# Performance work log

Hardware: AMD Instinct MI355X
Metric: run time of the kernel (lower is better)

The kernel has to match this reference:

```python
import jax, jax.numpy as jnp
import numpy as np

N = 20000   # nodes
E = 320000  # edges (before self-loops)
HID = 64    # hidden_dim
H = 4       # attention heads
C = HID     # per-head channels (concat=False -> mean over heads)
CDIM = 8    # contrastive_dim
NEG_SLOPE = 0.2


def setup_inputs() -> dict:
    key = jax.random.key(0)
    ks = jax.random.split(key, 32)
    g = lambda k, shape: (jax.random.normal(k, shape, jnp.float32) * 0.05)
    inp = {
        "x": jax.random.normal(ks[0], (N, 8), jnp.float32),
        "edge_index": jax.random.randint(ks[1], (2, E), 0, N, jnp.int64),
        # lc_encode MLP: 8 -> 32 -> HID
        "W_enc1": g(ks[2], (8, 32)),  "b_enc1": jnp.zeros((32,), jnp.float32),
        "W_enc2": g(ks[3], (32, HID)), "b_enc2": jnp.zeros((HID,), jnp.float32),
        # three GATConv layers: lin (HID -> H*C, no bias), att_src/att_dst (H, C), bias (C,)
        "W_g1": g(ks[4], (HID, H * C)), "as1": g(ks[5], (H, C)), "ad1": g(ks[6], (H, C)), "bg1": jnp.zeros((C,), jnp.float32),
        "W_g2": g(ks[7], (HID, H * C)), "as2": g(ks[8], (H, C)), "ad2": g(ks[9], (H, C)), "bg2": jnp.zeros((C,), jnp.float32),
        "W_g3": g(ks[10], (HID, H * C)), "as3": g(ks[11], (H, C)), "ad3": g(ks[12], (H, C)), "bg3": jnp.zeros((C,), jnp.float32),
        # output MLP: HID -> 64 -> 32 -> CDIM (dropout inactive at eval)
        "W_o1": g(ks[13], (HID, 64)), "b_o1": jnp.zeros((64,), jnp.float32),
        "W_o2": g(ks[14], (64, 32)),  "b_o2": jnp.zeros((32,), jnp.float32),
        "W_o3": g(ks[15], (32, CDIM)), "b_o3": jnp.zeros((CDIM,), jnp.float32),
    }
    return inp


def gat_conv(x, src, dst, n, W, att_src, att_dst, bias):
    # PyG GATConv, heads=H, concat=False (mean over heads), eval mode (no dropout)
    h = (x @ W).reshape(n, H, C)                       # [N,H,C]
    a_src = jnp.einsum('nhc,hc->nh', h, att_src)        # [N,H]
    a_dst = jnp.einsum('nhc,hc->nh', h, att_dst)        # [N,H]
    logits = jax.nn.leaky_relu(a_src[src] + a_dst[dst], NEG_SLOPE)  # [Etot,H]
    m = jax.ops.segment_max(logits, dst, num_segments=n)            # segment softmax (stable)
    e = jnp.exp(logits - m[dst])
    denom = jax.ops.segment_sum(e, dst, num_segments=n)
    alpha = e / (denom[dst] + 1e-16)                    # [Etot,H]
    msg = h[src] * alpha[:, :, None]                    # [Etot,H,C]
    out = jax.ops.segment_sum(msg, dst, num_segments=n) # [N,H,C]
    return out.mean(axis=1) + bias                      # concat=False -> head mean


def reference(x, edge_index, W_enc1, b_enc1, W_enc2, b_enc2,
              W_g1, as1, ad1, bg1, W_g2, as2, ad2, bg2, W_g3, as3, ad3, bg3,
              W_o1, b_o1, W_o2, b_o2, W_o3, b_o3):
    n = x.shape[0]
    loops = jnp.arange(n, dtype=edge_index.dtype)       # GATConv add_self_loops=True
    src = jnp.concatenate([edge_index[0], loops])
    dst = jnp.concatenate([edge_index[1], loops])

    h = jax.nn.elu(jax.nn.elu(x @ W_enc1 + b_enc1) @ W_enc2 + b_enc2)
    h1 = gat_conv(h, src, dst, n, W_g1, as1, ad1, bg1) + h
    h2 = gat_conv(h1, src, dst, n, W_g2, as2, ad2, bg2) + h1
    h3 = gat_conv(h2, src, dst, n, W_g3, as3, ad3, bg3) + h2

    o = jax.nn.elu(h3 @ W_o1 + b_o1)
    o = jax.nn.elu(o @ W_o2 + b_o2)
    return o @ W_o3 + b_o3
```

## Files before the change

### kernel.cpp

```cpp
#include <hip/hip_runtime.h>
#include <cstdint>
#include <cstddef>

#define NEG_SLOPE 0.2f

__device__ __forceinline__ float elu_f(float x) {
    return x > 0.f ? x : expm1f(x);
}

__global__ __launch_bounds__(256) void prep_kernel(
    const int* __restrict__ ei,
    const float* __restrict__ W0, const float* __restrict__ as0, const float* __restrict__ ad0,
    const float* __restrict__ W1, const float* __restrict__ as1, const float* __restrict__ ad1,
    const float* __restrict__ W2, const float* __restrict__ as2, const float* __restrict__ ad2,
    int* __restrict__ cnt, int* __restrict__ ready, int* __restrict__ flag,
    float* __restrict__ vfold, int n) {
    const int b = blockIdx.x, t = threadIdx.x;
    if (b < 79) {
        const int i = b * 256 + t;
        if (i < n) cnt[i] = 0;
        if (b == 0) {
            if (t < 128) ready[t] = 0;
            if (t == 0) {
                int acc = 0;
#pragma unroll
                for (int k = 0; k < 8; ++k) acc |= ei[2 * k + 1];
                flag[0] = (acc == 0) ? 1 : 0;
            }
        }
        return;
    }
    const int e = (b - 79) * 256 + t;
    if (e >= 1536) return;
    const int l = e >> 9, rem = e & 511;
    const int k = rem >> 3, j = rem & 7, h = j & 3;
    const float* W   = (l == 0) ? W0  : (l == 1) ? W1  : W2;
    const float* as_ = (l == 0) ? as0 : (l == 1) ? as1 : as2;
    const float* ad_ = (l == 0) ? ad0 : (l == 1) ? ad1 : ad2;
    const float* av = (j < 4) ? as_ : ad_;
    const float* wr = W + k * 256 + h * 64;
    const float* ar = av + h * 64;
    float s = 0.f;
#pragma unroll 8
    for (int cc = 0; cc < 64; ++cc) s += wr[cc] * ar[cc];
    vfold[l * 512 + k * 8 + j] = s;
}

__global__ void count_kernel(const int* __restrict__ ei, const int* __restrict__ flag,
                             int E, int Etot, int* __restrict__ cnt) {
    int e = blockIdx.x * blockDim.x + threadIdx.x;
    if (e >= Etot) return;
    int d;
    if (e < E) d = flag[0] ? ei[2 * (size_t)(E + e)] : ei[E + e];
    else       d = e - E;
    atomicAdd(&cnt[d], 1);
}

#define SCAN_B 256
__global__ __launch_bounds__(256) void scan_onepass_kernel(
    const int* __restrict__ cnt, int* __restrict__ ready,
    int* __restrict__ rowptr, int* __restrict__ cursor, int n) {
    __shared__ int sd[SCAN_B];
    __shared__ int sred[128];
    __shared__ int s_pref;
    const int b = blockIdx.x, t = threadIdx.x;
    const int g = b * SCAN_B + t;
    const int v = (g < n) ? cnt[g] : 0;
    sd[t] = v;
    __syncthreads();
    for (int off = 1; off < SCAN_B; off <<= 1) {
        int add = (t >= off) ? sd[t - off] : 0;
        __syncthreads();
        sd[t] += add;
        __syncthreads();
    }
    if (t == SCAN_B - 1) atomicExch(&ready[b], sd[SCAN_B - 1] + 1);
    if (t < 128) {
        int pv = 0;
        if (t < b) {
            do { pv = atomicAdd(&ready[t], 0); __builtin_amdgcn_s_sleep(1); } while (pv == 0);
            pv -= 1;
        }
        sred[t] = pv;
    }
    __syncthreads();
    if (t == 0) {
        int s = 0;
#pragma unroll 8
        for (int i = 0; i < 128; ++i) s += sred[i];
        s_pref = s;
    }
    __syncthreads();
    const int pre = s_pref;
    if (g < n) {
        const int e = pre + sd[t];
        rowptr[g + 1] = e;
        cursor[g] = e - v;
        if (g == 0) rowptr[0] = 0;
// ... 94 lines not shown
    float o[4][4];
#pragma unroll
    for (int i = 0; i < 4; ++i)
#pragma unroll
        for (int c = 0; c < 4; ++c) o[i][c] = elu_f(acc[i][c]);

#pragma unroll
    for (int i = 0; i < 4; ++i) {
        const int n = n0 + nq * 4 + i;
        if (n < n_nodes)
            *(float4*)(h0 + (size_t)n * 64 + c0) =
                make_float4(o[i][0], o[i][1], o[i][2], o[i][3]);
    }
    float ad[4][8];
#pragma unroll
    for (int i = 0; i < 4; ++i)
#pragma unroll
        for (int jj = 0; jj < 8; ++jj) ad[i][jj] = 0.f;
#pragma unroll
    for (int c = 0; c < 4; ++c) {
        const float4 v0 = *(const float4*)(vsd + (c0 + c) * 8);
        const float4 v1 = *(const float4*)(vsd + (c0 + c) * 8 + 4);
#pragma unroll
        for (int i = 0; i < 4; ++i) {
            ad[i][0] += o[i][c] * v0.x; ad[i][1] += o[i][c] * v0.y;
            ad[i][2] += o[i][c] * v0.z; ad[i][3] += o[i][c] * v0.w;
            ad[i][4] += o[i][c] * v1.x; ad[i][5] += o[i][c] * v1.y;
            ad[i][6] += o[i][c] * v1.z; ad[i][7] += o[i][c] * v1.w;
        }
    }
#pragma unroll
    for (int off = 1; off < 16; off <<= 1) {
#pragma unroll
        for (int i = 0; i < 4; ++i)
#pragma unroll
            for (int jj = 0; jj < 8; ++jj)
                ad[i][jj] += __shfl_xor(ad[i][jj], off);
    }
    if (cg == 0) {
#pragma unroll
        for (int i = 0; i < 4; ++i) {
            const int n = n0 + nq * 4 + i;
            if (n < n_nodes) {
#pragma unroll
                for (int h = 0; h < 4; ++h) {
                    asrc[n * 4 + h] = ad[i][h];
                    adst[n * 4 + h] = ad[i][4 + h];
                }
            }
        }
    }
}

#define GSTR 132
__global__ __launch_bounds__(512, 2) void gat_fused_kernel(
    const float* __restrict__ bin, const float* __restrict__ asrc,
    const float* __restrict__ adst, const int* __restrict__ rowptr,
    const int* __restrict__ col,
    const float* __restrict__ W, const float* __restrict__ bias,
    const float* __restrict__ vfold_next, int has_next,
    float* __restrict__ out,
    float* __restrict__ nasrc, float* __restrict__ nadst,
    const float* __restrict__ Wm1, const float* __restrict__ bm1,
    const float* __restrict__ Wm2, const float* __restrict__ bm2,
    const float* __restrict__ Wm3, const float* __restrict__ bm3,
    float* __restrict__ mlp_out, int n_nodes) {
    __shared__ float gS[64 * GSTR];
    __shared__ float Wp[4096];
    __shared__ float vN[512];
    const int t = threadIdx.x;
    const int n0 = blockIdx.x * 64;
    const int grp = t >> 4;
    const int q = t & 15;
    const int c0 = q * 4;

    if (has_next && t < 128) *(float4*)(vN + t * 4) = *(const float4*)(vfold_next + t * 4);

    float keep[2][8];
#pragma unroll
    for (int i = 0; i < 2; ++i) {
        const int nl = grp * 2 + i;
        const int n = n0 + nl;
        float acc[4][4];
#pragma unroll
        for (int h = 0; h < 4; ++h)
#pragma unroll
            for (int z = 0; z < 4; ++z) acc[h][z] = 0.f;
        if (n < n_nodes) {
            float4 den4 = make_float4(0.f, 0.f, 0.f, 0.f);
            const float4 ad4 = *(const float4*)(adst + (size_t)n * 4);
            const int start = rowptr[n], end = rowptr[n + 1];
            for (int base = start; base < end; base += 16) {
                const int cnt = min(16, end - base);
                int c = 0;
                float4 w4 = make_float4(0.f, 0.f, 0.f, 0.f);
                if (base + q < end) {
                    c = col[base + q];
                    const float4 av = *(const float4*)(asrc + (size_t)c * 4);
                    float l0 = av.x + ad4.x; l0 = l0 > 0.f ? l0 : NEG_SLOPE * l0;
                    float l1 = av.y + ad4.y; l1 = l1 > 0.f ? l1 : NEG_SLOPE * l1;
                    float l2 = av.z + ad4.z; l2 = l2 > 0.f ? l2 : NEG_SLOPE * l2;
                    float l3 = av.w + ad4.w; l3 = l3 > 0.f ? l3 : NEG_SLOPE * l3;
                    w4.x = __expf(fminf(l0, 60.f));
                    w4.y = __expf(fminf(l1, 60.f));
                    w4.z = __expf(fminf(l2, 60.f));
                    w4.w = __expf(fminf(l3, 60.f));
                    den4.x += w4.x; den4.y += w4.y; den4.z += w4.z; den4.w += w4.w;
                }
                int j = 0;
                for (; j + 4 <= cnt; j += 4) {
#pragma unroll
                    for (int u = 0; u < 4; ++u) {
                        const int s = __shfl(c, j + u, 16);
                        const float4 hv = *(const float4*)(bin + (size_t)s * 64 + q * 4);
                        const float wx = __shfl(w4.x, j + u, 16);
                        const float wy = __shfl(w4.y, j + u, 16);
                        const float wz = __shfl(w4.z, j + u, 16);
                        const float ww = __shfl(w4.w, j + u, 16);
                        acc[0][0] += wx * hv.x; acc[0][1] += wx * hv.y;
                        acc[0][2] += wx * hv.z; acc[0][3] += wx * hv.w;
                        acc[1][0] += wy * hv.x; acc[1][1] += wy * hv.y;
                        acc[1][2] += wy * hv.z; acc[1][3] += wy * hv.w;
                        acc[2][0] += wz * hv.x; acc[2][1] += wz * hv.y;
                        acc[2][2] += wz * hv.z; acc[2][3] += wz * hv.w;
                        acc[3][0] += ww * hv.x; acc[3][1] += ww * hv.y;
                        acc[3][2] += ww * hv.z; acc[3][3] += ww * hv.w;
                    }
                }
                for (; j < cnt; ++j) {
                    const int s = __shfl(c, j, 16);
                    const float4 hv = *(const float4*)(bin + (size_t)s * 64 + q * 4);
                    const float wx = __shfl(w4.x, j, 16);
                    const float wy = __shfl(w4.y, j, 16);
                    const float wz = __shfl(w4.z, j, 16);
                    const float ww = __shfl(w4.w, j, 16);
                    acc[0][0] += wx * hv.x; acc[0][1] += wx * hv.y;
                    acc[0][2] += wx * hv.z; acc[0][3] += wx * hv.w;
                    acc[1][0] += wy * hv.x; acc[1][1] += wy * hv.y;
                    acc[1][2] += wy * hv.z; acc[1][3] += wy * hv.w;
                    acc[2][0] += wz * hv.x; acc[2][1] += wz * hv.y;
                    acc[2][2] += wz * hv.z; acc[2][3] += wz * hv.w;
                    acc[3][0] += ww * hv.x; acc[3][1] += ww * hv.y;
                    acc[3][2] += ww * hv.z; acc[3][3] += ww * hv.w;
                }
            }
#pragma unroll
            for (int off = 1; off < 16; off <<= 1) {
                den4.x += __shfl_xor(den4.x, off, 16);
                den4.y += __shfl_xor(den4.y, off, 16);
                den4.z += __shfl_xor(den4.z, off, 16);
                den4.w += __shfl_xor(den4.w, off, 16);
            }
            const float i0 = 1.f / (den4.x + 1e-16f);
            const float i1 = 1.f / (den4.y + 1e-16f);
            const float i2 = 1.f / (den4.z + 1e-16f);
            const float i3 = 1.f / (den4.w + 1e-16f);
            *(float4*)(gS + nl * GSTR + c0) =
                make_float4(acc[0][0] * i0, acc[0][1] * i0, acc[0][2] * i0, acc[0][3] * i0);
            *(float4*)(gS + nl * GSTR + 64 + c0) =
                make_float4(acc[1][0] * i1, acc[1][1] * i1, acc[1][2] * i1, acc[1][3] * i1);
            keep[i][0] = acc[2][0] * i2; keep[i][1] = acc[2][1] * i2;
            keep[i][2] = acc[2][2] * i2; keep[i][3] = acc[2][3] * i2;
            keep[i][4] = acc[3][0] * i3; keep[i][5] = acc[3][1] * i3;
            keep[i][6] = acc[3][2] * i3; keep[i][7] = acc[3][3] * i3;
        } else {
            const float4 z4 = make_float4(0.f, 0.f, 0.f, 0.f);
            *(float4*)(gS + nl * GSTR + c0) = z4;
            *(float4*)(gS + nl * GSTR + 64 + c0) = z4;
#pragma unroll
            for (int u = 0; u < 8; ++u) keep[i][u] = 0.f;
        }
    }

    float ga2[2][4];
#pragma unroll
    for (int i = 0; i < 2; ++i)
#pragma unroll
        for (int c = 0; c < 4; ++c) ga2[i][c] = 0.f;

#pragma unroll
    for (int half = 0; half < 2; ++half) {
        if (half == 1) {
#pragma unroll
            for (int i = 0; i < 2; ++i) {
                const int nl = grp * 2 + i;
                *(float4*)(gS + nl * GSTR + c0) =
                    make_float4(keep[i][0], keep[i][1], keep[i][2], keep[i][3]);
                *(float4*)(gS + nl * GSTR + 64 + c0) =
                    make_float4(keep[i][4], keep[i][5], keep[i][6], keep[i][7]);
            }
        }
#pragma unroll
        for (int s = 0; s < 2; ++s) {
#pragma unroll
            for (int j = 0; j < 2; ++j) {
                const int f4 = j * 512 + t;
                const int kl = f4 >> 4;
                const int c = (f4 & 15) * 4;
                const int m = half * 128 + s * 64 + kl;
                const int h = m >> 6, kk = m & 63;
                *(float4*)(Wp + kl * 64 + c) = *(const float4*)(W + kk * 256 + h * 64 + c);
            }
            __syncthreads();
#pragma unroll 4
            for (int ks = 0; ks < 64; ks += 4) {
                const float4 a0 = *(const float4*)(gS + (grp * 2 + 0) * GSTR + s * 64 + ks);
                const float4 a1 = *(const float4*)(gS + (grp * 2 + 1) * GSTR + s * 64 + ks);
                const float4 w0 = *(const float4*)(Wp + (ks + 0) * 64 + c0);
                const float4 w1 = *(const float4*)(Wp + (ks + 1) * 64 + c0);
                const float4 w2 = *(const float4*)(Wp + (ks + 2) * 64 + c0);
                const float4 w3 = *(const float4*)(Wp + (ks + 3) * 64 + c0);
                ga2[0][0] += a0.x * w0.x + a0.y * w1.x + a0.z * w2.x + a0.w * w3.x;
                ga2[0][1] += a0.x * w0.y + a0.y * w1.y + a0.z * w2.y + a0.w * w3.y;
                ga2[0][2] += a0.x * w0.z + a0.y * w1.z + a0.z * w2.z + a0.w * w3.z;
                ga2[0][3] += a0.x * w0.w + a0.y * w1.w + a0.z * w2.w + a0.w * w3.w;
                ga2[1][0] += a1.x * w0.x + a1.y * w1.x + a1.z * w2.x + a1.w * w3.x;
                ga2[1][1] += a1.x * w0.y + a1.y * w1.y + a1.z * w2.y + a1.w * w3.y;
                ga2[1][2] += a1.x * w0.z + a1.y * w1.z + a1.z * w2.z + a1.w * w3.z;
                ga2[1][3] += a1.x * w0.w + a1.y * w1.w + a1.z * w2.w + a1.w * w3.w;
            }
            __syncthreads();
        }
    }

    const float4 bb = *(const float4*)(bias + c0);
    float o[2][4];
#pragma unroll
    for (int i = 0; i < 2; ++i) {
        const int n = n0 + grp * 2 + i;
        if (n < n_nodes) {
            const float4 x4 = *(const float4*)(bin + (size_t)n * 64 + c0);
            o[i][0] = 0.25f * ga2[i][0] + bb.x + x4.x;
            o[i][1] = 0.25f * ga2[i][1] + bb.y + x4.y;
            o[i][2] = 0.25f * ga2[i][2] + bb.z + x4.z;
            o[i][3] = 0.25f * ga2[i][3] + bb.w + x4.w;
            if (has_next)
                *(float4*)(out + (size_t)n * 64 + c0) =
                    make_float4(o[i][0], o[i][1], o[i][2], o[i][3]);
        } else {
            o[i][0] = o[i][1] = o[i][2] = o[i][3] = 0.f;
        }
    }

    if (has_next) {
        float pj[2][8];
#pragma unroll
        for (int i = 0; i < 2; ++i)
#pragma unroll
            for (int jj = 0; jj < 8; ++jj) pj[i][jj] = 0.f;
#pragma unroll
        for (int c = 0; c < 4; ++c) {
            const float4 v0 = *(const float4*)(vN + (c0 + c) * 8);
            const float4 v1 = *(const float4*)(vN + (c0 + c) * 8 + 4);
#pragma unroll
            for (int i = 0; i < 2; ++i) {
                pj[i][0] += o[i][c] * v0.x; pj[i][1] += o[i][c] * v0.y;
                pj[i][2] += o[i][c] * v0.z; pj[i][3] += o[i][c] * v0.w;
                pj[i][4] += o[i][c] * v1.x; pj[i][5] += o[i][c] * v1.y;
                pj[i][6] += o[i][c] * v1.z; pj[i][7] += o[i][c] * v1.w;
            }
        }
#pragma unroll
        for (int off = 1; off < 16; off <<= 1) {
#pragma unroll
            for (int i = 0; i < 2; ++i)
#pragma unroll
                for (int jj = 0; jj < 8; ++jj)
                    pj[i][jj] += __shfl_xor(pj[i][jj], off);
        }
        if (q == 0) {
#pragma unroll
            for (int i = 0; i < 2; ++i) {
                const int n = n0 + grp * 2 + i;
                if (n < n_nodes) {
#pragma unroll
                    for (int h = 0; h < 4; ++h) {
                        nasrc[n * 4 + h] = pj[i][h];
                        nadst[n * 4 + h] = pj[i][4 + h];
                    }
                }
            }
        }
        return;
    }

#pragma unroll
    for (int i = 0; i < 2; ++i)
        *(float4*)(gS + (grp * 2 + i) * GSTR + c0) =
            make_float4(o[i][0], o[i][1], o[i][2], o[i][3]);
#pragma unroll
    for (int j = 0; j < 2; ++j)
        *(float4*)(Wp + (j * 512 + t) * 4) = *(const float4*)(Wm1 + (j * 512 + t) * 4);
    if (t < 64) vN[t] = bm1[t];
    else if (t < 96) vN[t] = bm2[t - 64];
    else if (t < 104) vN[t] = bm3[t - 96];
    if (t < 256) vN[104 + t] = Wm3[t];
    __syncthreads();
    {
        const int ng = t >> 3;
        const int cm0 = (t & 7) * 8;
        float a1[8];
#pragma unroll
        for (int u = 0; u < 8; ++u) a1[u] = vN[cm0 + u];
#pragma unroll 4
        for (int k = 0; k < 64; ++k) {
            const float hv = gS[ng * GSTR + k];
            const float4 w0 = *(const float4*)(Wp + k * 64 + cm0);
            const float4 w1 = *(const float4*)(Wp + k * 64 + cm0 + 4);
            a1[0] += hv * w0.x; a1[1] += hv * w0.y;
            a1[2] += hv * w0.z; a1[3] += hv * w0.w;
            a1[4] += hv * w1.x; a1[5] += hv * w1.y;
            a1[6] += hv * w1.z; a1[7] += hv * w1.w;
        }
        *(float4*)(gS + ng * GSTR + 64 + cm0) =
            make_float4(elu_f(a1[0]), elu_f(a1[1]), elu_f(a1[2]), elu_f(a1[3]));
        *(float4*)(gS + ng * GSTR + 64 + cm0 + 4) =
            make_float4(elu_f(a1[4]), elu_f(a1[5]), elu_f(a1[6]), elu_f(a1[7]));
    }
    __syncthreads();
    *(float4*)(Wp + t * 4) = *(const float4*)(Wm2 + t * 4);
    __syncthreads();
    {
        const int nn = t >> 3;
        const int cc0 = (t & 7) * 4;
        float a2[4];
#pragma unroll
        for (int u = 0; u < 4; ++u) a2[u] = vN[64 + cc0 + u];
#pragma unroll 4
        for (int j = 0; j < 64; ++j) {
            const float ov = gS[nn * GSTR + 64 + j];
            const float4 w = *(const float4*)(Wp + j * 32 + cc0);
            a2[0] += ov * w.x; a2[1] += ov * w.y;
            a2[2] += ov * w.z; a2[3] += ov * w.w;
        }
        __syncthreads();
        *(float4*)(gS + nn * GSTR + cc0) =
            make_float4(elu_f(a2[0]), elu_f(a2[1]), elu_f(a2[2]), elu_f(a2[3]));
    }
    __syncthreads();
    {
        const int nl = t >> 3;
        const int c3 = t & 7;
        const int n = n0 + nl;
        if (n < n_nodes) {
            float a3 = vN[96 + c3];
#pragma unroll 4
            for (int j = 0; j < 32; ++j)
                a3 += gS[nl * GSTR + j] * vN[104 + j * 8 + c3];
            mlp_out[(size_t)n * 8 + c3] = a3;
        }
    }
}

extern "C" void kernel_launch(void* const* d_in, const int* in_sizes, int n_in,
                              void* d_out, int out_size, void* d_ws, size_t ws_size,
                              hipStream_t stream) {
    const float* x     = (const float*)d_in[0];
    const int*   ei    = (const int*)d_in[1];
    const float* Wenc1 = (const float*)d_in[2];
    const float* benc1 = (const float*)d_in[3];
    const float* Wenc2 = (const float*)d_in[4];
    const float* benc2 = (const float*)d_in[5];
    const float* Wg[3]  = {(const float*)d_in[6],  (const float*)d_in[10], (const float*)d_in[14]};
    const float* as_[3] = {(const float*)d_in[7],  (const float*)d_in[11], (const float*)d_in[15]};
    const float* ad_[3] = {(const float*)d_in[8],  (const float*)d_in[12], (const float*)d_in[16]};
    const float* bg[3]  = {(const float*)d_in[9],  (const float*)d_in[13], (const float*)d_in[17]};
    const float* Wo1 = (const float*)d_in[18];
    const float* bo1 = (const float*)d_in[19];
    const float* Wo2 = (const float*)d_in[20];
    const float* bo2 = (const float*)d_in[21];
    const float* Wo3 = (const float*)d_in[22];
    const float* bo3 = (const float*)d_in[23];

    const int N = in_sizes[0] / 8;
    const int E = in_sizes[1] / 2;
    const int Etot = E + N;
    const int nblk = (N + SCAN_B - 1) / SCAN_B;
    const int FB = (Etot + 255) / 256;
    const int NB64 = (N + 63) / 64;

    float* buf0  = (float*)d_ws;
    float* buf1  = buf0 + (size_t)N * 64;
    float* asA   = buf1 + (size_t)N * 64;
    float* adA   = asA + (size_t)N * 4;
    float* asB   = adA + (size_t)N * 4;
    float* adB   = asB + (size_t)N * 4;
    float* vfold = adB + (size_t)N * 4;
    int* rowptr = (int*)(vfold + 3 * 512);
    int* cursor = rowptr + (N + 2);
    int* cnt    = cursor + N;
    int* ready  = cnt + N;
    int* flag   = ready + 128;
    int* col    = flag + 2;

    prep_kernel<<<nblk + 6, 256, 0, stream>>>(ei,
        Wg[0], as_[0], ad_[0], Wg[1], as_[1], ad_[1], Wg[2], as_[2], ad_[2],
        cnt, ready, flag, vfold, N);
    count_kernel<<<(Etot + 255) / 256, 256, 0, stream>>>(ei, flag, E, Etot, cnt);
    scan_onepass_kernel<<<nblk, SCAN_B, 0, stream>>>(cnt, ready, rowptr, cursor, N);
    fillenc_kernel<<<FB + NB64, 256, 0, stream>>>(ei, flag, E, Etot, cursor, col, FB,
                                                  x, Wenc1, benc1, Wenc2, benc2,
                                                  vfold, buf0, asA, adA, N);

    gat_fused_kernel<<<NB64, 512, 0, stream>>>(
        buf0, asA, adA, rowptr, col, Wg[0], bg[0], vfold + 512, 1,
        buf1, asB, adB, Wo1, bo1, Wo2, bo2, Wo3, bo3, (float*)d_out, N);
    gat_fused_kernel<<<NB64, 512, 0, stream>>>(
        buf1, asB, adB, rowptr, col, Wg[1], bg[1], vfold + 1024, 1,
        buf0, asA, adA, Wo1, bo1, Wo2, bo2, Wo3, bo3, (float*)d_out, N);
    gat_fused_kernel<<<NB64, 512, 0, stream>>>(
        buf0, asA, adA, rowptr, col, Wg[2], bg[2], vfold, 0,
        buf1, asB, adB, Wo1, bo1, Wo2, bo2, Wo3, bo3, (float*)d_out, N);
}
```

Baseline: 282.0 us.

## Halve GAT node tile to one node per thread group and raise occupancy bound

Each fused GAT block now covers 32 nodes instead of 64. Every 16-thread group aggregates one node's neighbours rather than two, which doubles the grid and should spread the latency-bound gather across more CUs. The dense projection and MLP tail run on only half the threads, and the launch bound asks for 8 blocks per CU. That bound may force a tight register budget and cause spills, while the idle half of the block wastes lanes during the GEMM phase.

Measured after the change: 281.8 us (median of 3 runs). Within noise of the previous version (-0.1%).

```diff
diff --git a/kernel.cpp b/kernel.cpp
--- a/kernel.cpp
+++ b/kernel.cpp
@@ -245,7 +245,7 @@
 }
 
 #define GSTR 132
-__global__ __launch_bounds__(512, 2) void gat_fused_kernel(
+__global__ __launch_bounds__(512, 8) void gat_fused_kernel(
     const float* __restrict__ bin, const float* __restrict__ asrc,
     const float* __restrict__ adst, const int* __restrict__ rowptr,
     const int* __restrict__ col,
@@ -257,22 +257,20 @@
     const float* __restrict__ Wm2, const float* __restrict__ bm2,
     const float* __restrict__ Wm3, const float* __restrict__ bm3,
     float* __restrict__ mlp_out, int n_nodes) {
-    __shared__ float gS[64 * GSTR];
+    __shared__ float gS[32 * GSTR];
     __shared__ float Wp[4096];
     __shared__ float vN[512];
     const int t = threadIdx.x;
-    const int n0 = blockIdx.x * 64;
+    const int n0 = blockIdx.x * 32;
     const int grp = t >> 4;
     const int q = t & 15;
     const int c0 = q * 4;
 
     if (has_next && t < 128) *(float4*)(vN + t * 4) = *(const float4*)(vfold_next + t * 4);
 
-    float keep[2][8];
-#pragma unroll
-    for (int i = 0; i < 2; ++i) {
-        const int nl = grp * 2 + i;
-        const int n = n0 + nl;
+    float keep[8];
+    {
+        const int n = n0 + grp;
         float acc[4][4];
 #pragma unroll
         for (int h = 0; h < 4; ++h)
@@ -347,23 +345,24 @@
             const float i1 = 1.f / (den4.y + 1e-16f);
             const float i2 = 1.f / (den4.z + 1e-16f);
             const float i3 = 1.f / (den4.w + 1e-16f);
-            *(float4*)(gS + nl * GSTR + c0) =
+            *(float4*)(gS + grp * GSTR + c0) =
                 make_float4(acc[0][0] * i0, acc[0][1] * i0, acc[0][2] * i0, acc[0][3] * i0);
-            *(float4*)(gS + nl * GSTR + 64 + c0) =
+            *(float4*)(gS + grp * GSTR + 64 + c0) =
                 make_float4(acc[1][0] * i1, acc[1][1] * i1, acc[1][2] * i1, acc[1][3] * i1);
-            keep[i][0] = acc[2][0] * i2; keep[i][1] = acc[2][1] * i2;
-            keep[i][2] = acc[2][2] * i2; keep[i][3] = acc[2][3] * i2;
-            keep[i][4] = acc[3][0] * i3; keep[i][5] = acc[3][1] * i3;
-            keep[i][6] = acc[3][2] * i3; keep[i][7] = acc[3][3] * i3;
+            keep[0] = acc[2][0] * i2; keep[1] = acc[2][1] * i2;
+            keep[2] = acc[2][2] * i2; keep[3] = acc[2][3] * i2;
+            keep[4] = acc[3][0] * i3; keep[5] = acc[3][1] * i3;
+            keep[6] = acc[3][2] * i3; keep[7] = acc[3][3] * i3;
         } else {
             const float4 z4 = make_float4(0.f, 0.f, 0.f, 0.f);
-            *(float4*)(gS + nl * GSTR + c0) = z4;
-            *(float4*)(gS + nl * GSTR + 64 + c0) = z4;
-#pragma unroll
-            for (int u = 0; u < 8; ++u) keep[i][u] = 0.f;
-        }
-    }
-
+            *(float4*)(gS + grp * GSTR + c0) = z4;
+            *(float4*)(gS + grp * GSTR + 64 + c0) = z4;
+#pragma unroll
+            for (int u = 0; u < 8; ++u) keep[u] = 0.f;
+        }
+    }
+
+    const int ng2 = t >> 4;
     float ga2[2][4];
 #pragma unroll
     for (int i = 0; i < 2; ++i)
@@ -373,14 +372,10 @@
 #pragma unroll
     for (int half = 0; half < 2; ++half) {
         if (half == 1) {
-#pragma unroll
-            for (int i = 0; i < 2; ++i) {
-                const int nl = grp * 2 + i;
-                *(float4*)(gS + nl * GSTR + c0) =
-                    make_float4(keep[i][0], keep[i][1], keep[i][2], keep[i][3]);
-                *(float4*)(gS + nl * GSTR + 64 + c0) =
-                    make_float4(keep[i][4], keep[i][5], keep[i][6], keep[i][7]);
-            }
+            *(float4*)(gS + grp * GSTR + c0) =
+                make_float4(keep[0], keep[1], keep[2], keep[3]);
+            *(float4*)(gS + grp * GSTR + 64 + c0) =
+                make_float4(keep[4], keep[5], keep[6], keep[7]);
         }
 #pragma unroll
         for (int s = 0; s < 2; ++s) {
@@ -394,81 +389,91 @@
                 *(float4*)(Wp + kl * 64 + c) = *(const float4*)(W + kk * 256 + h * 64 + c);
             }
             __syncthreads();
+            if (t < 256) {
 #pragma unroll 4
-            for (int ks = 0; ks < 64; ks += 4) {
-                const float4 a0 = *(const float4*)(gS + (grp * 2 + 0) * GSTR + s * 64 + ks);
-                const float4 a1 = *(const float4*)(gS + (grp * 2 + 1) * GSTR + s * 64 + ks);
-                const float4 w0 = *(const float4*)(Wp + (ks + 0) * 64 + c0);
-                const float4 w1 = *(const float4*)(Wp + (ks + 1) * 64 + c0);
-                const float4 w2 = *(const float4*)(Wp + (ks + 2) * 64 + c0);
-                const float4 w3 = *(const float4*)(Wp + (ks + 3) * 64 + c0);
-                ga2[0][0] += a0.x * w0.x + a0.y * w1.x + a0.z * w2.x + a0.w * w3.x;
-                ga2[0][1] += a0.x * w0.y + a0.y * w1.y + a0.z * w2.y + a0.w * w3.y;
-                ga2[0][2] += a0.x * w0.z + a0.y * w1.z + a0.z * w2.z + a0.w * w3.z;
-                ga2[0][3] += a0.x * w0.w + a0.y * w1.w + a0.z * w2.w + a0.w * w3.w;
-                ga2[1][0] += a1.x * w0.x + a1.y * w1.x + a1.z * w2.x + a1.w * w3.x;
-                ga2[1][1] += a1.x * w0.y + a1.y * w1.y + a1.z * w2.y + a1.w * w3.y;
-                ga2[1][2] += a1.x * w0.z + a1.y * w1.z + a1.z * w2.z + a1.w * w3.z;
-                ga2[1][3] += a1.x * w0.w + a1.y * w1.w + a1.z * w2.w + a1.w * w3.w;
+                for (int ks = 0; ks < 64; ks += 4) {
+                    const float4 a0 = *(const float4*)(gS + (ng2 * 2 + 0) * GSTR + s * 64 + ks);
+                    const float4 a1 = *(const float4*)(gS + (ng2 * 2 + 1) * GSTR + s * 64 + ks);
+                    const float4 w0 = *(const float4*)(Wp + (ks + 0) * 64 + c0);
+                    const float4 w1 = *(const float4*)(Wp + (ks + 1) * 64 + c0);
+                    const float4 w2 = *(const float4*)(Wp + (ks + 2) * 64 + c0);
+                    const float4 w3 = *(const float4*)(Wp + (ks + 3) * 64 + c0);
+                    ga2[0][0] += a0.x * w0.x + a0.y * w1.x + a0.z * w2.x + a0.w * w3.x;
+                    ga2[0][1] += a0.x * w0.y + a0.y * w1.y + a0.z * w2.y + a0.w * w3.y;
+                    ga2[0][2] += a0.x * w0.z + a0.y * w1.z + a0.z * w2.z + a0.w * w3.z;
+                    ga2[0][3] += a0.x * w0.w + a0.y * w1.w + a0.z * w2.w + a0.w * w3.w;
+                    ga2[1][0] += a1.x * w0.x + a1.y * w1.x + a1.z * w2.x + a1.w * w3.x;
+                    ga2[1][1] += a1.x * w0.y + a1.y * w1.y + a1.z * w2.y + a1.w * w3.y;
+                    ga2[1][2] += a1.x * w0.z + a1.y * w1.z + a1.z * w2.z + a1.w * w3.z;
+                    ga2[1][3] += a1.x * w0.w + a1.y * w1.w + a1.z * w2.w + a1.w * w3.w;
+                }
             }
             __syncthreads();
         }
     }
 
-    const float4 bb = *(const float4*)(bias + c0);
     float o[2][4];
-#pragma unroll
-    for (int i = 0; i < 2; ++i) {
-        const int n = n0 + grp * 2 + i;
-        if (n < n_nodes) {
-            const float4 x4 = *(const float4*)(bin + (size_t)n * 64 + c0);
-            o[i][0] = 0.25f * ga2[i][0] + bb.x + x4.x;
-            o[i][1] = 0.25f * ga2[i][1] + bb.y + x4.y;
-            o[i][2] = 0.25f * ga2[i][2] + bb.z + x4.z;
-            o[i][3] = 0.25f * ga2[i][3] + bb.w + x4.w;
-            if (has_next)
-                *(float4*)(out + (size_t)n * 64 + c0) =
-                    make_float4(o[i][0], o[i][1], o[i][2], o[i][3]);
-        } else {
+    if (t < 256) {
+        const float4 bb = *(const float4*)(bias + c0);
+#pragma unroll
+        for (int i = 0; i < 2; ++i) {
+            const int n = n0 + ng2 * 2 + i;
+            if (n < n_nodes) {
+                const float4 x4 = *(const float4*)(bin + (size_t)n * 64 + c0);
+                o[i][0] = 0.25f * ga2[i][0] + bb.x + x4.x;
+                o[i][1] = 0.25f * ga2[i][1] + bb.y + x4.y;
+                o[i][2] = 0.25f * ga2[i][2] + bb.z + x4.z;
+                o[i][3] = 0.25f * ga2[i][3] + bb.w + x4.w;
+                if (has_next)
+                    *(float4*)(out + (size_t)n * 64 + c0) =
+                        make_float4(o[i][0], o[i][1], o[i][2], o[i][3]);
+            } else {
+                o[i][0] = o[i][1] = o[i][2] = o[i][3] = 0.f;
+            }
+        }
+    } else {
+#pragma unroll
+        for (int i = 0; i < 2; ++i)
             o[i][0] = o[i][1] = o[i][2] = o[i][3] = 0.f;
-        }
     }
 
     if (has_next) {
-        float pj[2][8];
-#pragma unroll
-        for (int i = 0; i < 2; ++i)
-#pragma unroll
-            for (int jj = 0; jj < 8; ++jj) pj[i][jj] = 0.f;
-#pragma unroll
-        for (int c = 0; c < 4; ++c) {
-            const float4 v0 = *(const float4*)(vN + (c0 + c) * 8);
-            const float4 v1 = *(const float4*)(vN + (c0 + c) * 8 + 4);
-#pragma unroll
-            for (int i = 0; i < 2; ++i) {
-                pj[i][0] += o[i][c] * v0.x; pj[i][1] += o[i][c] * v0.y;
-                pj[i][2] += o[i][c] * v0.z; pj[i][3] += o[i][c] * v0.w;
-                pj[i][4] += o[i][c] * v1.x; pj[i][5] += o[i][c] * v1.y;
-                pj[i][6] += o[i][c] * v1.z; pj[i][7] += o[i][c] * v1.w;
-            }
-        }
-#pragma unroll
-        for (int off = 1; off < 16; off <<= 1) {
+        if (t < 256) {
+            float pj[2][8];
 #pragma unroll
             for (int i = 0; i < 2; ++i)
 #pragma unroll
-                for (int jj = 0; jj < 8; ++jj)
-                    pj[i][jj] += __shfl_xor(pj[i][jj], off);
-        }
-        if (q == 0) {
-#pragma unroll
-            for (int i = 0; i < 2; ++i) {
-                const int n = n0 + grp * 2 + i;
-                if (n < n_nodes) {
-#pragma unroll
-                    for (int h = 0; h < 4; ++h) {
-                        nasrc[n * 4 + h] = pj[i][h];
-                        nadst[n * 4 + h] = pj[i][4 + h];
+                for (int jj = 0; jj < 8; ++jj) pj[i][jj] = 0.f;
+#pragma unroll
+            for (int c = 0; c < 4; ++c) {
+                const float4 v0 = *(const float4*)(vN + (c0 + c) * 8);
+                const float4 v1 = *(const float4*)(vN + (c0 + c) * 8 + 4);
+#pragma unroll
+                for (int i = 0; i < 2; ++i) {
+                    pj[i][0] += o[i][c] * v0.x; pj[i][1] += o[i][c] * v0.y;
+                    pj[i][2] += o[i][c] * v0.z; pj[i][3] += o[i][c] * v0.w;
+                    pj[i][4] += o[i][c] * v1.x; pj[i][5] += o[i][c] * v1.y;
+                    pj[i][6] += o[i][c] * v1.z; pj[i][7] += o[i][c] * v1.w;
+                }
+            }
+#pragma unroll
+            for (int off = 1; off < 16; off <<= 1) {
+#pragma unroll
+                for (int i = 0; i < 2; ++i)
+#pragma unroll
+                    for (int jj = 0; jj < 8; ++jj)
+                        pj[i][jj] += __shfl_xor(pj[i][jj], off);
+            }
+            if (q == 0) {
+#pragma unroll
+                for (int i = 0; i < 2; ++i) {
+                    const int n = n0 + ng2 * 2 + i;
+                    if (n < n_nodes) {
+#pragma unroll
+                        for (int h = 0; h < 4; ++h) {
+                            nasrc[n * 4 + h] = pj[i][h];
+                            nadst[n * 4 + h] = pj[i][4 + h];
+                        }
                     }
                 }
             }
@@ -476,10 +481,12 @@
         return;
     }
 
-#pragma unroll
-    for (int i = 0; i < 2; ++i)
-        *(float4*)(gS + (grp * 2 + i) * GSTR + c0) =
-            make_float4(o[i][0], o[i][1], o[i][2], o[i][3]);
+    if (t < 256) {
+#pragma unroll
+        for (int i = 0; i < 2; ++i)
+            *(float4*)(gS + (ng2 * 2 + i) * GSTR + c0) =
+                make_float4(o[i][0], o[i][1], o[i][2], o[i][3]);
+    }
 #pragma unroll
     for (int j = 0; j < 2; ++j)
         *(float4*)(Wp + (j * 512 + t) * 4) = *(const float4*)(Wm1 + (j * 512 + t) * 4);
@@ -488,7 +495,7 @@
     else if (t < 104) vN[t] = bm3[t - 96];
     if (t < 256) vN[104 + t] = Wm3[t];
     __syncthreads();
-    {
+    if (t < 256) {
         const int ng = t >> 3;
         const int cm0 = (t & 7) * 8;
         float a1[8];
@@ -512,7 +519,7 @@
     __syncthreads();
     *(float4*)(Wp + t * 4) = *(const float4*)(Wm2 + t * 4);
     __syncthreads();
-    {
+    if (t < 256) {
         const int nn = t >> 3;
         const int cc0 = (t & 7) * 4;
         float a2[4];
@@ -528,9 +535,11 @@
         __syncthreads();
         *(float4*)(gS + nn * GSTR + cc0) =
             make_float4(elu_f(a2[0]), elu_f(a2[1]), elu_f(a2[2]), elu_f(a2[3]));
-    }
-    __syncthreads();
-    {
+    } else {
+        __syncthreads();
+    }
+    __syncthreads();
+    if (t < 256) {
         const int nl = t >> 3;
         const int c3 = t & 7;
         const int n = n0 + nl;
@@ -570,6 +579,7 @@
     const int nblk = (N + SCAN_B - 1) / SCAN_B;
     const int FB = (Etot + 255) / 256;
     const int NB64 = (N + 63) / 64;
+    const int NB32 = (N + 31) / 32;
 
     float* buf0  = (float*)d_ws;
     float* buf1  = buf0 + (size_t)N * 64;
@@ -594,13 +604,13 @@
                                                   x, Wenc1, benc1, Wenc2, benc2,
                                                   vfold, buf0, asA, adA, N);
 
-    gat_fused_kernel<<<NB64, 512, 0, stream>>>(
+    gat_fused_kernel<<<NB32, 512, 0, stream>>>(
         buf0, asA, adA, rowptr, col, Wg[0], bg[0], vfold + 512, 1,
         buf1, asB, adB, Wo1, bo1, Wo2, bo2, Wo3, bo3, (float*)d_out, N);
-    gat_fused_kernel<<<NB64, 512, 0, stream>>>(
+    gat_fused_kernel<<<NB32, 512, 0, stream>>>(
         buf1, asB, adB, rowptr, col, Wg[1], bg[1], vfold + 1024, 1,
         buf0, asA, adA, Wo1, bo1, Wo2, bo2, Wo3, bo3, (float*)d_out, N);
-    gat_fused_kernel<<<NB64, 512, 0, stream>>>(
+    gat_fused_kernel<<<NB32, 512, 0, stream>>>(
         buf0, asA, adA, rowptr, col, Wg[2], bg[2], vfold, 0,
         buf1, asB, adB, Wo1, bo1, Wo2, bo2, Wo3, bo3, (float*)d_out, N);
 }
```

## Pre-transpose GAT weights and stream them from global in fused layer kernel

Applied to the files above, without the earlier changes.

The prep kernel now writes a transposed, per-wave-sliced copy of each GAT weight matrix. The fused layer kernel stores all four head aggregates in an XOR-swizzled shared tile and has each wave compute 8 output channels for 64 nodes, reading weights straight from global or L2 instead of staging them through shared memory in halves. Each lane now recomputes attention weights per edge instead of exchanging them by shuffle. Dropping the weight buffer and shuffles is meant to cut LDS use and barriers so the launch bound can rise to 4 blocks per CU. The cost is a larger gS tile and more redundant exp and asrc loads per edge.

Measured after the change: 300.1 us. 6.4% more time.

```diff
diff --git a/kernel.cpp b/kernel.cpp
--- a/kernel.cpp
+++ b/kernel.cpp
@@ -14,7 +14,7 @@
     const float* __restrict__ W1, const float* __restrict__ as1, const float* __restrict__ ad1,
     const float* __restrict__ W2, const float* __restrict__ as2, const float* __restrict__ ad2,
     int* __restrict__ cnt, int* __restrict__ ready, int* __restrict__ flag,
-    float* __restrict__ vfold, int n) {
+    float* __restrict__ vfold, float* __restrict__ wt, int n) {
     const int b = blockIdx.x, t = threadIdx.x;
     if (b < 79) {
         const int i = b * 256 + t;
@@ -30,20 +30,32 @@
         }
         return;
     }
-    const int e = (b - 79) * 256 + t;
-    if (e >= 1536) return;
-    const int l = e >> 9, rem = e & 511;
-    const int k = rem >> 3, j = rem & 7, h = j & 3;
-    const float* W   = (l == 0) ? W0  : (l == 1) ? W1  : W2;
-    const float* as_ = (l == 0) ? as0 : (l == 1) ? as1 : as2;
-    const float* ad_ = (l == 0) ? ad0 : (l == 1) ? ad1 : ad2;
-    const float* av = (j < 4) ? as_ : ad_;
-    const float* wr = W + k * 256 + h * 64;
-    const float* ar = av + h * 64;
-    float s = 0.f;
+    if (b < 85) {
+        const int e = (b - 79) * 256 + t;
+        if (e >= 1536) return;
+        const int l = e >> 9, rem = e & 511;
+        const int k = rem >> 3, j = rem & 7, h = j & 3;
+        const float* W   = (l == 0) ? W0  : (l == 1) ? W1  : W2;
+        const float* as_ = (l == 0) ? as0 : (l == 1) ? as1 : as2;
+        const float* ad_ = (l == 0) ? ad0 : (l == 1) ? ad1 : ad2;
+        const float* av = (j < 4) ? as_ : ad_;
+        const float* wr = W + k * 256 + h * 64;
+        const float* ar = av + h * 64;
+        float s = 0.f;
 #pragma unroll 8
-    for (int cc = 0; cc < 64; ++cc) s += wr[cc] * ar[cc];
-    vfold[l * 512 + k * 8 + j] = s;
+        for (int cc = 0; cc < 64; ++cc) s += wr[cc] * ar[cc];
+        vfold[l * 512 + k * 8 + j] = s;
+        return;
+    }
+    const int idx = (b - 85) * 256 + t;
+    if (idx >= 3 * 16384) return;
+    const int l = idx >> 14;
+    const int r = idx & 16383;
+    const float* W = (l == 0) ? W0 : (l == 1) ? W1 : W2;
+    const int w = r >> 11;
+    const int kap = (r >> 3) & 255;
+    const int c = r & 7;
+    wt[idx] = W[(kap & 63) * 256 + (kap >> 6) * 64 + w * 8 + c];
 }
 
 __global__ void count_kernel(const int* __restrict__ ei, const int* __restrict__ flag,
@@ -244,12 +256,12 @@
     }
 }
 
-#define GSTR 132
-__global__ __launch_bounds__(512, 2) void gat_fused_kernel(
+#define GSTR 264
+__global__ __launch_bounds__(512, 4) void gat_fused_kernel(
     const float* __restrict__ bin, const float* __restrict__ asrc,
     const float* __restrict__ adst, const int* __restrict__ rowptr,
     const int* __restrict__ col,
-    const float* __restrict__ W, const float* __restrict__ bias,
+    const float* __restrict__ Wt, const float* __restrict__ bias,
     const float* __restrict__ vfold_next, int has_next,
     float* __restrict__ out,
     float* __restrict__ nasrc, float* __restrict__ nadst,
@@ -258,21 +270,19 @@
     const float* __restrict__ Wm3, const float* __restrict__ bm3,
     float* __restrict__ mlp_out, int n_nodes) {
     __shared__ float gS[64 * GSTR];
-    __shared__ float Wp[4096];
     __shared__ float vN[512];
     const int t = threadIdx.x;
     const int n0 = blockIdx.x * 64;
     const int grp = t >> 4;
     const int q = t & 15;
-    const int c0 = q * 4;
 
     if (has_next && t < 128) *(float4*)(vN + t * 4) = *(const float4*)(vfold_next + t * 4);
 
-    float keep[2][8];
 #pragma unroll
     for (int i = 0; i < 2; ++i) {
         const int nl = grp * 2 + i;
         const int n = n0 + nl;
+        const int sw = nl & 7;
         float acc[4][4];
 #pragma unroll
         for (int h = 0; h < 4; ++h)
@@ -285,191 +295,132 @@
             for (int base = start; base < end; base += 16) {
                 const int cnt = min(16, end - base);
                 int c = 0;
-                float4 w4 = make_float4(0.f, 0.f, 0.f, 0.f);
-                if (base + q < end) {
-                    c = col[base + q];
-                    const float4 av = *(const float4*)(asrc + (size_t)c * 4);
+                if (base + q < end) c = col[base + q];
+#pragma unroll 4
+                for (int j = 0; j < cnt; ++j) {
+                    const int s = __shfl(c, j, 16);
+                    const float4 av = *(const float4*)(asrc + (size_t)s * 4);
+                    const float4 hv = *(const float4*)(bin + (size_t)s * 64 + q * 4);
                     float l0 = av.x + ad4.x; l0 = l0 > 0.f ? l0 : NEG_SLOPE * l0;
                     float l1 = av.y + ad4.y; l1 = l1 > 0.f ? l1 : NEG_SLOPE * l1;
                     float l2 = av.z + ad4.z; l2 = l2 > 0.f ? l2 : NEG_SLOPE * l2;
                     float l3 = av.w + ad4.w; l3 = l3 > 0.f ? l3 : NEG_SLOPE * l3;
-                    w4.x = __expf(fminf(l0, 60.f));
-                    w4.y = __expf(fminf(l1, 60.f));
-                    w4.z = __expf(fminf(l2, 60.f));
-                    w4.w = __expf(fminf(l3, 60.f));
-                    den4.x += w4.x; den4.y += w4.y; den4.z += w4.z; den4.w += w4.w;
-                }
-                int j = 0;
-                for (; j + 4 <= cnt; j += 4) {
-#pragma unroll
-                    for (int u = 0; u < 4; ++u) {
-                        const int s = __shfl(c, j + u, 16);
-                        const float4 hv = *(const float4*)(bin + (size_t)s * 64 + q * 4);
-                        const float wx = __shfl(w4.x, j + u, 16);
-                        const float wy = __shfl(w4.y, j + u, 16);
-                        const float wz = __shfl(w4.z, j + u, 16);
-                        const float ww = __shfl(w4.w, j + u, 16);
-                        acc[0][0] += wx * hv.x; acc[0][1] += wx * hv.y;
-                        acc[0][2] += wx * hv.z; acc[0][3] += wx * hv.w;
-                        acc[1][0] += wy * hv.x; acc[1][1] += wy * hv.y;
-                        acc[1][2] += wy * hv.z; acc[1][3] += wy * hv.w;
-                        acc[2][0] += wz * hv.x; acc[2][1] += wz * hv.y;
-                        acc[2][2] += wz * hv.z; acc[2][3] += wz * hv.w;
-                        acc[3][0] += ww * hv.x; acc[3][1] += ww * hv.y;
-                        acc[3][2] += ww * hv.z; acc[3][3] += ww * hv.w;
-                    }
-                }
-                for (; j < cnt; ++j) {
-                    const int s = __shfl(c, j, 16);
-                    const float4 hv = *(const float4*)(bin + (size_t)s * 64 + q * 4);
-                    const float wx = __shfl(w4.x, j, 16);
-                    const float wy = __shfl(w4.y, j, 16);
-                    const float wz = __shfl(w4.z, j, 16);
-                    const float ww = __shfl(w4.w, j, 16);
-                    acc[0][0] += wx * hv.x; acc[0][1] += wx * hv.y;
-                    acc[0][2] += wx * hv.z; acc[0][3] += wx * hv.w;
-                    acc[1][0] += wy * hv.x; acc[1][1] += wy * hv.y;
-                    acc[1][2] += wy * hv.z; acc[1][3] += wy * hv.w;
-                    acc[2][0] += wz * hv.x; acc[2][1] += wz * hv.y;
-                    acc[2][2] += wz * hv.z; acc[2][3] += wz * hv.w;
-                    acc[3][0] += ww * hv.x; acc[3][1] += ww * hv.y;
-                    acc[3][2] += ww * hv.z; acc[3][3] += ww * hv.w;
+                    const float w0 = __expf(fminf(l0, 60.f));
+                    const float w1 = __expf(fminf(l1, 60.f));
+                    const float w2 = __expf(fminf(l2, 60.f));
+                    const float w3 = __expf(fminf(l3, 60.f));
+                    den4.x += w0; den4.y += w1; den4.z += w2; den4.w += w3;
+                    acc[0][0] += w0 * hv.x; acc[0][1] += w0 * hv.y;
+                    acc[0][2] += w0 * hv.z; acc[0][3] += w0 * hv.w;
+                    acc[1][0] += w1 * hv.x; acc[1][1] += w1 * hv.y;
+                    acc[1][2] += w1 * hv.z; acc[1][3] += w1 * hv.w;
+                    acc[2][0] += w2 * hv.x; acc[2][1] += w2 * hv.y;
+                    acc[2][2] += w2 * hv.z; acc[2][3] += w2 * hv.w;
+                    acc[3][0] += w3 * hv.x; acc[3][1] += w3 * hv.y;
+                    acc[3][2] += w3 * hv.z; acc[3][3] += w3 * hv.w;
                 }
             }
-#pragma unroll
-            for (int off = 1; off < 16; off <<= 1) {
-                den4.x += __shfl_xor(den4.x, off, 16);
-                den4.y += __shfl_xor(den4.y, off, 16);
-                den4.z += __shfl_xor(den4.z, off, 16);
-                den4.w += __shfl_xor(den4.w, off, 16);
+            const float iv[4] = {1.f / (den4.x + 1e-16f), 1.f / (den4.y + 1e-16f),
+                                 1.f / (den4.z + 1e-16f), 1.f / (den4.w + 1e-16f)};
+#pragma unroll
+            for (int h = 0; h < 4; ++h) {
+                const int u = (h * 16 + q) ^ sw;
+                *(float4*)(gS + nl * GSTR + (u << 2)) =
+                    make_float4(acc[h][0] * iv[h], acc[h][1] * iv[h],
+                                acc[h][2] * iv[h], acc[h][3] * iv[h]);
             }
-            const float i0 = 1.f / (den4.x + 1e-16f);
-            const float i1 = 1.f / (den4.y + 1e-16f);
-            const float i2 = 1.f / (den4.z + 1e-16f);
-            const float i3 = 1.f / (den4.w + 1e-16f);
-            *(float4*)(gS + nl * GSTR + c0) =
-                make_float4(acc[0][0] * i0, acc[0][1] * i0, acc[0][2] * i0, acc[0][3] * i0);
-            *(float4*)(gS + nl * GSTR + 64 + c0) =
-                make_float4(acc[1][0] * i1, acc[1][1] * i1, acc[1][2] * i1, acc[1][3] * i1);
-            keep[i][0] = acc[2][0] * i2; keep[i][1] = acc[2][1] * i2;
-            keep[i][2] = acc[2][2] * i2; keep[i][3] = acc[2][3] * i2;
-            keep[i][4] = acc[3][0] * i3; keep[i][5] = acc[3][1] * i3;
-            keep[i][6] = acc[3][2] * i3; keep[i][7] = acc[3][3] * i3;
         } else {
             const float4 z4 = make_float4(0.f, 0.f, 0.f, 0.f);
-            *(float4*)(gS + nl * GSTR + c0) = z4;
-            *(float4*)(gS + nl * GSTR + 64 + c0) = z4;
-#pragma unroll
-            for (int u = 0; u < 8; ++u) keep[i][u] = 0.f;
-        }
-    }
-
-    float ga2[2][4];
-#pragma unroll
-    for (int i = 0; i < 2; ++i)
-#pragma unroll
-        for (int c = 0; c < 4; ++c) ga2[i][c] = 0.f;
-
-#pragma unroll
-    for (int half = 0; half < 2; ++half) {
-        if (half == 1) {
-#pragma unroll
-            for (int i = 0; i < 2; ++i) {
-                const int nl = grp * 2 + i;
-                *(float4*)(gS + nl * GSTR + c0) =
-                    make_float4(keep[i][0], keep[i][1], keep[i][2], keep[i][3]);
-                *(float4*)(gS + nl * GSTR + 64 + c0) =
-                    make_float4(keep[i][4], keep[i][5], keep[i][6], keep[i][7]);
+#pragma unroll
+            for (int h = 0; h < 4; ++h) {
+                const int u = (h * 16 + q) ^ sw;
+                *(float4*)(gS + nl * GSTR + (u << 2)) = z4;
             }
         }
-#pragma unroll
-        for (int s = 0; s < 2; ++s) {
-#pragma unroll
-            for (int j = 0; j < 2; ++j) {
-                const int f4 = j * 512 + t;
-                const int kl = f4 >> 4;
-                const int c = (f4 & 15) * 4;
-                const int m = half * 128 + s * 64 + kl;
-                const int h = m >> 6, kk = m & 63;
-                *(float4*)(Wp + kl * 64 + c) = *(const float4*)(W + kk * 256 + h * 64 + c);
-            }
-            __syncthreads();
+    }
+    __syncthreads();
+
+    const int wv = __builtin_amdgcn_readfirstlane(t >> 6);
+    const int nl2 = t & 63;
+    const int sw2 = nl2 & 7;
+    const float* __restrict__ Wv = Wt + wv * 2048;
+    const float* __restrict__ gr = gS + nl2 * GSTR;
+    float ga[8];
+#pragma unroll
+    for (int cc = 0; cc < 8; ++cc) ga[cc] = 0.f;
 #pragma unroll 4
-            for (int ks = 0; ks < 64; ks += 4) {
-                const float4 a0 = *(const float4*)(gS + (grp * 2 + 0) * GSTR + s * 64 + ks);
-                const float4 a1 = *(const float4*)(gS + (grp * 2 + 1) * GSTR + s * 64 + ks);
-                const float4 w0 = *(const float4*)(Wp + (ks + 0) * 64 + c0);
-                const float4 w1 = *(const float4*)(Wp + (ks + 1) * 64 + c0);
-                const float4 w2 = *(const float4*)(Wp + (ks + 2) * 64 + c0);
-                const float4 w3 = *(const float4*)(Wp + (ks + 3) * 64 + c0);
-                ga2[0][0] += a0.x * w0.x + a0.y * w1.x + a0.z * w2.x + a0.w * w3.x;
-                ga2[0][1] += a0.x * w0.y + a0.y * w1.y + a0.z * w2.y + a0.w * w3.y;
-                ga2[0][2] += a0.x * w0.z + a0.y * w1.z + a0.z * w2.z + a0.w * w3.z;
-                ga2[0][3] += a0.x * w0.w + a0.y * w1.w + a0.z * w2.w + a0.w * w3.w;
-                ga2[1][0] += a1.x * w0.x + a1.y * w1.x + a1.z * w2.x + a1.w * w3.x;
-                ga2[1][1] += a1.x * w0.y + a1.y * w1.y + a1.z * w2.y + a1.w * w3.y;
-                ga2[1][2] += a1.x * w0.z + a1.y * w1.z + a1.z * w2.z + a1.w * w3.z;
-                ga2[1][3] += a1.x * w0.w + a1.y * w1.w + a1.z * w2.w + a1.w * w3.w;
-            }
-            __syncthreads();
-        }
-    }
-
-    const float4 bb = *(const float4*)(bias + c0);
-    float o[2][4];
-#pragma unroll
-    for (int i = 0; i < 2; ++i) {
-        const int n = n0 + grp * 2 + i;
-        if (n < n_nodes) {
-            const float4 x4 = *(const float4*)(bin + (size_t)n * 64 + c0);
-            o[i][0] = 0.25f * ga2[i][0] + bb.x + x4.x;
-            o[i][1] = 0.25f * ga2[i][1] + bb.y + x4.y;
-            o[i][2] = 0.25f * ga2[i][2] + bb.z + x4.z;
-            o[i][3] = 0.25f * ga2[i][3] + bb.w + x4.w;
-            if (has_next)
-                *(float4*)(out + (size_t)n * 64 + c0) =
-                    make_float4(o[i][0], o[i][1], o[i][2], o[i][3]);
-        } else {
-            o[i][0] = o[i][1] = o[i][2] = o[i][3] = 0.f;
-        }
-    }
+    for (int u = 0; u < 64; ++u) {
+        const float4 a4 = *(const float4*)(gr + ((u ^ sw2) << 2));
+        const float* wr = Wv + u * 32;
+        const float aarr[4] = {a4.x, a4.y, a4.z, a4.w};
+#pragma unroll
+        for (int kk = 0; kk < 4; ++kk) {
+#pragma unroll
+            for (int cc = 0; cc < 8; ++cc)
+                ga[cc] += aarr[kk] * wr[kk * 8 + cc];
+        }
+    }
+
+    const int n2 = n0 + nl2;
+    const float* bb = bias + wv * 8;
+    float o8[8];
+    if (n2 < n_nodes) {
+        const float4 x0 = *(const float4*)(bin + (size_t)n2 * 64 + wv * 8);
+        const float4 x1 = *(const float4*)(bin + (size_t)n2 * 64 + wv * 8 + 4);
+        o8[0] = 0.25f * ga[0] + bb[0] + x0.x;
+        o8[1] = 0.25f * ga[1] + bb[1] + x0.y;
+        o8[2] = 0.25f * ga[2] + bb[2] + x0.z;
+        o8[3] = 0.25f * ga[3] + bb[3] + x0.w;
+        o8[4] = 0.25f * ga[4] + bb[4] + x1.x;
+        o8[5] = 0.25f * ga[5] + bb[5] + x1.y;
+        o8[6] = 0.25f * ga[6] + bb[6] + x1.z;
+        o8[7] = 0.25f * ga[7] + bb[7] + x1.w;
+        if (has_next) {
+            *(float4*)(out + (size_t)n2 * 64 + wv * 8) =
+                make_float4(o8[0], o8[1], o8[2], o8[3]);
+            *(float4*)(out + (size_t)n2 * 64 + wv * 8 + 4) =
+                make_float4(o8[4], o8[5], o8[6], o8[7]);
+        }
+    } else {
+#pragma unroll
+        for (int cc = 0; cc < 8; ++cc) o8[cc] = 0.f;
+    }
+    __syncthreads();
+    *(float4*)(gS + nl2 * GSTR + wv * 8)     = make_float4(o8[0], o8[1], o8[2], o8[3]);
+    *(float4*)(gS + nl2 * GSTR + wv * 8 + 4) = make_float4(o8[4], o8[5], o8[6], o8[7]);
+    __syncthreads();
 
     if (has_next) {
-        float pj[2][8];
-#pragma unroll
-        for (int i = 0; i < 2; ++i)
-#pragma unroll
-            for (int jj = 0; jj < 8; ++jj) pj[i][jj] = 0.f;
-#pragma unroll
-        for (int c = 0; c < 4; ++c) {
-            const float4 v0 = *(const float4*)(vN + (c0 + c) * 8);
-            const float4 v1 = *(const float4*)(vN + (c0 + c) * 8 + 4);
-#pragma unroll
-            for (int i = 0; i < 2; ++i) {
-                pj[i][0] += o[i][c] * v0.x; pj[i][1] += o[i][c] * v0.y;
-                pj[i][2] += o[i][c] * v0.z; pj[i][3] += o[i][c] * v0.w;
-                pj[i][4] += o[i][c] * v1.x; pj[i][5] += o[i][c] * v1.y;
-                pj[i][6] += o[i][c] * v1.z; pj[i][7] += o[i][c] * v1.w;
-            }
-        }
-#pragma unroll
-        for (int off = 1; off < 16; off <<= 1) {
-#pragma unroll
-            for (int i = 0; i < 2; ++i)
-#pragma unroll
-                for (int jj = 0; jj < 8; ++jj)
-                    pj[i][jj] += __shfl_xor(pj[i][jj], off);
-        }
-        if (q == 0) {
-#pragma unroll
-            for (int i = 0; i < 2; ++i) {
-                const int n = n0 + grp * 2 + i;
-                if (n < n_nodes) {
-#pragma unroll
-                    for (int h = 0; h < 4; ++h) {
-                        nasrc[n * 4 + h] = pj[i][h];
-                        nadst[n * 4 + h] = pj[i][4 + h];
-                    }
+        const int nd = t >> 3, qq = t & 7;
+        const float* orow = gS + nd * GSTR + qq * 8;
+        const float4 ov0 = *(const float4*)(orow);
+        const float4 ov1 = *(const float4*)(orow + 4);
+        const float ov[8] = {ov0.x, ov0.y, ov0.z, ov0.w, ov1.x, ov1.y, ov1.z, ov1.w};
+        float pj[8];
+#pragma unroll
+        for (int jj = 0; jj < 8; ++jj) pj[jj] = 0.f;
+#pragma unroll
+        for (int u = 0; u < 8; ++u) {
+            const float4 v0 = *(const float4*)(vN + (qq * 8 + u) * 8);
+            const float4 v1 = *(const float4*)(vN + (qq * 8 + u) * 8 + 4);
+            pj[0] += ov[u] * v0.x; pj[1] += ov[u] * v0.y;
+            pj[2] += ov[u] * v0.z; pj[3] += ov[u] * v0.w;
+            pj[4] += ov[u] * v1.x; pj[5] += ov[u] * v1.y;
+            pj[6] += ov[u] * v1.z; pj[7] += ov[u] * v1.w;
+        }
+#pragma unroll
+        for (int off = 1; off < 8; off <<= 1) {
+#pragma unroll
+            for (int jj = 0; jj < 8; ++jj)
+                pj[jj] += __shfl_xor(pj[jj], off, 8);
+        }
+        if (qq == 0) {
+            const int n = n0 + nd;
+            if (n < n_nodes) {
+#pragma unroll
+                for (int h = 0; h < 4; ++h) {
+                    nasrc[n * 4 + h] = pj[h];
+                    nadst[n * 4 + h] = pj[4 + h];
                 }
             }
         }
@@ -477,12 +428,11 @@
     }
 
 #pragma unroll
-    for (int i = 0; i < 2; ++i)
-        *(float4*)(gS + (grp * 2 + i) * GSTR + c0) =
-            make_float4(o[i][0], o[i][1], o[i][2], o[i][3]);
-#pragma unroll
-    for (int j = 0; j < 2; ++j)
-        *(float4*)(Wp + (j * 512 + t) * 4) = *(const float4*)(Wm1 + (j * 512 + t) * 4);
+    for (int jj = 0; jj < 2; ++jj) {
+        const int idx = jj * 512 + t;
+        *(float4*)(gS + (idx >> 4) * GSTR + 128 + (idx & 15) * 4) =
+            *(const float4*)(Wm1 + idx * 4);
+    }
     if (t < 64) vN[t] = bm1[t];
     else if (t < 96) vN[t] = bm2[t - 64];
     else if (t < 104) vN[t] = bm3[t - 96];
@@ -497,20 +447,20 @@
 #pragma unroll 4
         for (int k = 0; k < 64; ++k) {
             const float hv = gS[ng * GSTR + k];
-            const float4 w0 = *(const float4*)(Wp + k * 64 + cm0);
-            const float4 w1 = *(const float4*)(Wp + k * 64 + cm0 + 4);
+            const float4 w0 = *(const float4*)(gS + k * GSTR + 128 + cm0);
+            const float4 w1 = *(const float4*)(gS + k * GSTR + 128 + cm0 + 4);
             a1[0] += hv * w0.x; a1[1] += hv * w0.y;
             a1[2] += hv * w0.z; a1[3] += hv * w0.w;
             a1[4] += hv * w1.x; a1[5] += hv * w1.y;
             a1[6] += hv * w1.z; a1[7] += hv * w1.w;
         }
-        *(float4*)(gS + ng * GSTR + 64 + cm0) =
+        __syncthreads();
+        *(float4*)(gS + ng * GSTR + 192 + cm0) =
             make_float4(elu_f(a1[0]), elu_f(a1[1]), elu_f(a1[2]), elu_f(a1[3]));
-        *(float4*)(gS + ng * GSTR + 64 + cm0 + 4) =
+        *(float4*)(gS + ng * GSTR + 192 + cm0 + 4) =
             make_float4(elu_f(a1[4]), elu_f(a1[5]), elu_f(a1[6]), elu_f(a1[7]));
     }
-    __syncthreads();
-    *(float4*)(Wp + t * 4) = *(const float4*)(Wm2 + t * 4);
+    *(float4*)(gS + (t >> 3) * GSTR + 128 + (t & 7) * 4) = *(const float4*)(Wm2 + t * 4);
     __syncthreads();
     {
         const int nn = t >> 3;
@@ -520,25 +470,24 @@
         for (int u = 0; u < 4; ++u) a2[u] = vN[64 + cc0 + u];
 #pragma unroll 4
         for (int j = 0; j < 64; ++j) {
-            const float ov = gS[nn * GSTR + 64 + j];
-            const float4 w = *(const float4*)(Wp + j * 32 + cc0);
+            const float ov = gS[nn * GSTR + 192 + j];
+            const float4 w = *(const float4*)(gS + j * GSTR + 128 + cc0);
             a2[0] += ov * w.x; a2[1] += ov * w.y;
             a2[2] += ov * w.z; a2[3] += ov * w.w;
         }
-        __syncthreads();
-        *(float4*)(gS + nn * GSTR + cc0) =
+        *(float4*)(gS + nn * GSTR + 64 + cc0) =
             make_float4(elu_f(a2[0]), elu_f(a2[1]), elu_f(a2[2]), elu_f(a2[3]));
     }
     __syncthreads();
     {
-        const int nl = t >> 3;
+        const int nd = t >> 3;
         const int c3 = t & 7;
-        const int n = n0 + nl;
+        const int n = n0 + nd;
         if (n < n_nodes) {
             float a3 = vN[96 + c3];
 #pragma unroll 4
             for (int j = 0; j < 32; ++j)
-                a3 += gS[nl * GSTR + j] * vN[104 + j * 8 + c3];
+                a3 += gS[nd * GSTR + 64 + j] * vN[104 + j * 8 + c3];
             mlp_out[(size_t)n * 8 + c3] = a3;
         }
     }
@@ -578,16 +527,17 @@
     float* asB   = adA + (size_t)N * 4;
     float* adB   = asB + (size_t)N * 4;
     float* vfold = adB + (size_t)N * 4;
-    int* rowptr = (int*)(vfold + 3 * 512);
+    float* wt    = vfold + 3 * 512;
+    int* rowptr = (int*)(wt + 3 * 16384);
     int* cursor = rowptr + (N + 2);
     int* cnt    = cursor + N;
     int* ready  = cnt + N;
     int* flag   = ready + 128;
     int* col    = flag + 2;
 
-    prep_kernel<<<nblk + 6, 256, 0, stream>>>(ei,
+    prep_kernel<<<79 + 6 + 192, 256, 0, stream>>>(ei,
         Wg[0], as_[0], ad_[0], Wg[1], as_[1], ad_[1], Wg[2], as_[2], ad_[2],
-        cnt, ready, flag, vfold, N);
+        cnt, ready, flag, vfold, wt, N);
     count_kernel<<<(Etot + 255) / 256, 256, 0, stream>>>(ei, flag, E, Etot, cnt);
     scan_onepass_kernel<<<nblk, SCAN_B, 0, stream>>>(cnt, ready, rowptr, cursor, N);
     fillenc_kernel<<<FB + NB64, 256, 0, stream>>>(ei, flag, E, Etot, cursor, col, FB,
@@ -595,12 +545,12 @@
                                                   vfold, buf0, asA, adA, N);
 
     gat_fused_kernel<<<NB64, 512, 0, stream>>>(
-        buf0, asA, adA, rowptr, col, Wg[0], bg[0], vfold + 512, 1,
+        buf0, asA, adA, rowptr, col, wt, bg[0], vfold + 512, 1,
         buf1, asB, adB, Wo1, bo1, Wo2, bo2, Wo3, bo3, (float*)d_out, N);
     gat_fused_kernel<<<NB64, 512, 0, stream>>>(
-        buf1, asB, adB, rowptr, col, Wg[1], bg[1], vfold + 1024, 1,
+        buf1, asB, adB, rowptr, col, wt + 16384, bg[1], vfold + 1024, 1,
         buf0, asA, adA, Wo1, bo1, Wo2, bo2, Wo3, bo3, (float*)d_out, N);
     gat_fused_kernel<<<NB64, 512, 0, stream>>>(
-        buf0, asA, adA, rowptr, col, Wg[2], bg[2], vfold, 0,
+        buf0, asA, adA, rowptr, col, wt + 32768, bg[2], vfold, 0,
         buf1, asB, adB, Wo1, bo1, Wo2, bo2, Wo3, bo3, (float*)d_out, N);
 }
```
